# Kernel optimization log

Hardware: AMD Instinct MI355X
Metric: run time of the kernel (lower is better)

The kernel has to match this reference:

```python
import jax, jax.numpy as jnp
import numpy as np

N_NODES = 50000
N_EDGES = 800000
NUM_GRAPHS = 512
D_IN = 64
D_H = 64
BN_EPS = 1e-5


def setup_inputs() -> dict:
    key = jax.random.key(0)
    ks = jax.random.split(key, 12)
    x = jax.random.normal(ks[0], (N_NODES, D_IN), dtype=jnp.float32)
    edge_index = jax.random.randint(ks[1], (2, N_EDGES), 0, N_NODES, dtype=jnp.int64)
    batch = jnp.sort(jax.random.randint(ks[2], (N_NODES,), 0, NUM_GRAPHS, dtype=jnp.int64))
    s1 = 1.0 / np.sqrt(D_IN)
    s2 = 1.0 / np.sqrt(D_H)
    s3 = 1.0 / np.sqrt(2 * D_H)
    W1 = jax.random.uniform(ks[3], (D_IN, D_H), jnp.float32, -s1, s1)
    b1 = jax.random.uniform(ks[4], (D_H,), jnp.float32, -s1, s1)
    gamma = jnp.ones((D_H,), jnp.float32)
    beta = jnp.zeros((D_H,), jnp.float32)
    W2 = jax.random.uniform(ks[5], (D_H, D_H), jnp.float32, -s2, s2)
    b2 = jax.random.uniform(ks[6], (D_H,), jnp.float32, -s2, s2)
    Wl1 = jax.random.uniform(ks[7], (2 * D_H, 2 * D_H), jnp.float32, -s3, s3)
    bl1 = jax.random.uniform(ks[8], (2 * D_H,), jnp.float32, -s3, s3)
    Wl2 = jax.random.uniform(ks[9], (2 * D_H, 1), jnp.float32, -s3, s3)
    bl2 = jax.random.uniform(ks[10], (1,), jnp.float32, -s3, s3)
    return {"x": x, "edge_index": edge_index, "batch": batch,
            "W1": W1, "b1": b1, "gamma": gamma, "beta": beta,
            "W2": W2, "b2": b2, "Wl1": Wl1, "bl1": bl1, "Wl2": Wl2, "bl2": bl2}


def reference(x, edge_index, batch, W1, b1, gamma, beta, W2, b2, Wl1, bl1, Wl2, bl2):
    src, dst = edge_index[0], edge_index[1]
    # GINConv with eps=0: (1+eps)*x_i + sum_{j->i} x_j
    agg = x + jax.ops.segment_sum(x[src], dst, num_segments=N_NODES)
    # MLP: Linear -> BatchNorm1d (training stats, biased var) -> ReLU -> Linear -> ReLU
    h = agg @ W1 + b1
    mean = jnp.mean(h, axis=0)
    var = jnp.var(h, axis=0)
    h = (h - mean) * jax.lax.rsqrt(var + BN_EPS) * gamma + beta
    h = jax.nn.relu(h)
    h = jax.nn.relu(h @ W2 + b2)
    # global add/max pooling per graph
    h_add = jax.ops.segment_sum(h, batch, num_segments=NUM_GRAPHS)
    h_max = jax.ops.segment_max(h, batch, num_segments=NUM_GRAPHS)
    g = jnp.concatenate((h_add, h_max), axis=1)  # [G, 2*D_H]
    g = jax.nn.relu(g @ Wl1 + bl1)
    logits = g @ Wl2 + bl2  # [G, 1]
    return (jax.nn.sigmoid(logits), logits)
```

## Files before the change

kernel.cpp:

```cpp
#include <hip/hip_runtime.h>
#include <hip/hip_bf16.h>

#define N_NODES 50000
#define N_EDGES 800000
#define NUM_GRAPHS 512
#define D 64
#define BN_EPS 1e-5f

#define BUK_SHIFT 7
#define BUK_SIZE 128
#define NBUK ((N_NODES + BUK_SIZE - 1) / BUK_SIZE)
#define CHUNK_A 4096
#define NBLK_A ((N_EDGES + CHUNK_A - 1) / CHUNK_A)
#define GBLK ((N_NODES + 63) / 64)
#define SBLK 256

__global__ __launch_bounds__(512) void k_zero(int* __restrict__ bcnt,
                                              int* __restrict__ offs) {
    int t = threadIdx.x;
    for (int j = t; j < NBUK; j += 512) bcnt[j] = 0;
    if (t == 0) offs[N_NODES] = N_EDGES;
}

__global__ __launch_bounds__(256) void k_bhist(const int* __restrict__ ei,
                                               int* __restrict__ bcnt) {
    __shared__ int h[NBUK];
    int t = threadIdx.x;
    for (int j = t; j < NBUK; j += 256) h[j] = 0;
    __syncthreads();
    int e0 = blockIdx.x * CHUNK_A;
#pragma unroll
    for (int i = 0; i < CHUNK_A / 256; i++) {
        int e = e0 + i * 256 + t;
        if (e < N_EDGES) atomicAdd(&h[ei[N_EDGES + e] >> BUK_SHIFT], 1);
    }
    __syncthreads();
    for (int j = t; j < NBUK; j += 256)
        if (h[j]) atomicAdd(&bcnt[j], h[j]);
}

__global__ __launch_bounds__(512) void k_bscan(const int* __restrict__ bcnt,
                                               int* __restrict__ boffs,
                                               int* __restrict__ gcur) {
    __shared__ int sm[512];
    int t = threadIdx.x;
    int v = (t < NBUK) ? bcnt[t] : 0;
    sm[t] = v;
    __syncthreads();
    for (int off = 1; off < 512; off <<= 1) {
        int a = sm[t];
        int u = (t >= off) ? sm[t - off] : 0;
        __syncthreads();
        sm[t] = a + u;
        __syncthreads();
    }
    if (t < NBUK) { int ex = sm[t] - v; boffs[t] = ex; gcur[t] = ex; }
    if (t == 0) boffs[NBUK] = N_EDGES;
}

__global__ __launch_bounds__(256) void k_binA(const int* __restrict__ ei,
                                              int* __restrict__ gcur,
                                              unsigned* __restrict__ pairs) {
    __shared__ int cnt[NBUK];
    __shared__ int base[NBUK];
    int t = threadIdx.x;
    for (int j = t; j < NBUK; j += 256) cnt[j] = 0;
    __syncthreads();
    int e0 = blockIdx.x * CHUNK_A;
    unsigned pd[CHUNK_A / 256];
    int loc[CHUNK_A / 256];
#pragma unroll
    for (int i = 0; i < CHUNK_A / 256; i++) {
        int e = e0 + i * 256 + t;
        pd[i] = 0xFFFFFFFFu;
        if (e < N_EDGES) {
            unsigned s = (unsigned)ei[e];
            unsigned d = (unsigned)ei[N_EDGES + e];
            pd[i] = (d << 16) | s;
            loc[i] = atomicAdd(&cnt[d >> BUK_SHIFT], 1);
        }
    }
    __syncthreads();
    for (int j = t; j < NBUK; j += 256)
        base[j] = cnt[j] ? atomicAdd(&gcur[j], cnt[j]) : 0;
    __syncthreads();
#pragma unroll
    for (int i = 0; i < CHUNK_A / 256; i++) {
        if (pd[i] != 0xFFFFFFFFu) {
            unsigned d = pd[i] >> 16;
            pairs[base[d >> BUK_SHIFT] + loc[i]] =
                ((d & (BUK_SIZE - 1)) << 16) | (pd[i] & 0xFFFFu);
        }
    }
}

__global__ __launch_bounds__(256) void k_sort(const unsigned* __restrict__ pairs,
                                              const int* __restrict__ boffs,
                                              int* __restrict__ offs,
                                              int* __restrict__ esrc) {
    __shared__ int cnt[BUK_SIZE];
    __shared__ int sm[BUK_SIZE];
    __shared__ int cur[BUK_SIZE];
    int b = blockIdx.x, t = threadIdx.x;
    int n0 = b << BUK_SHIFT;
    int nrows = min(BUK_SIZE, N_NODES - n0);
    int e0 = boffs[b], e1 = boffs[b + 1];
    int m = e1 - e0;
    if (t < BUK_SIZE) cnt[t] = 0;
    __syncthreads();
    for (int j = t; j < m; j += 256)
        atomicAdd(&cnt[pairs[e0 + j] >> 16], 1);
    __syncthreads();
    if (t < BUK_SIZE) sm[t] = cnt[t];
    __syncthreads();
    for (int off = 1; off < BUK_SIZE; off <<= 1) {
        int v = 0, u = 0;
        if (t < BUK_SIZE) { v = sm[t]; u = (t >= off) ? sm[t - off] : 0; }
        __syncthreads();
        if (t < BUK_SIZE) sm[t] = v + u;
        __syncthreads();
    }
    if (t < BUK_SIZE) {
        int ex = sm[t] - cnt[t];
        cur[t] = ex;
        if (t < nrows) offs[n0 + t] = e0 + ex;
    }
    __syncthreads();
    for (int j = t; j < m; j += 256) {
        unsigned p = pairs[e0 + j];
        int pos = atomicAdd(&cur[p >> 16], 1);
        esrc[e0 + pos] = (int)(p & 0xFFFFu);
    }
}

__global__ __launch_bounds__(256) void k_gather(const float* __restrict__ x,
                                                const int* __restrict__ offs,
                                                const int* __restrict__ esrc,
                                                float* __restrict__ agg) {
    int wid = (blockIdx.x * 256 + threadIdx.x) >> 6;
    int c = threadIdx.x & 63;
    if (wid >= N_NODES) return;
    int base = offs[wid];
    int end = offs[wid + 1];
    float acc = x[(size_t)wid * D + c];
    int i = base;
    for (; i + 3 < end; i += 4) {
        int s0 = esrc[i], s1 = esrc[i + 1], s2 = esrc[i + 2], s3 = esrc[i + 3];
        float v0 = x[(size_t)s0 * D + c];
        float v1 = x[(size_t)s1 * D + c];
        float v2 = x[(size_t)s2 * D + c];
        float v3 = x[(size_t)s3 * D + c];
        acc += v0; acc += v1; acc += v2; acc += v3;
    }
    for (; i < end; i++) acc += x[(size_t)esrc[i] * D + c];
    agg[(size_t)wid * D + c] = acc;
}

__global__ __launch_bounds__(256) void k_gemm1(const float* __restrict__ agg,
                                               const float* __restrict__ W1,
                                               const float* __restrict__ b1,
                                               float* __restrict__ h) {
    __shared__ float xs[64][65];
    int blk = blockIdx.x, t = threadIdx.x;
    int r0 = blk * 64;
    const float4* a4 = (const float4*)(agg + (size_t)r0 * D);
    for (int i = t; i < 1024; i += 256) {
        float4 v = a4[i];
        int row = i >> 4, q = (i & 15) * 4;
        xs[row][q] = v.x; xs[row][q + 1] = v.y;
        xs[row][q + 2] = v.z; xs[row][q + 3] = v.w;
    }
    __syncthreads();
    int lane = t & 63, chunk = t >> 6;
    int r = r0 + lane;
    int c0 = chunk * 16;
    float acc[16];
#pragma unroll
    for (int j = 0; j < 16; j++) acc[j] = b1[c0 + j];
#pragma unroll 4
    for (int k = 0; k < D; k++) {
        float v = xs[lane][k];
#pragma unroll
        for (int j = 0; j < 16; j++)
            acc[j] += v * W1[k * D + c0 + j];
    }
    if (r < N_NODES) {
        float* hp = h + (size_t)r * D + c0;
#pragma unroll
        for (int j4 = 0; j4 < 4; j4++) {
            float4 o;
            o.x = acc[j4 * 4]; o.y = acc[j4 * 4 + 1];
            o.z = acc[j4 * 4 + 2]; o.w = acc[j4 * 4 + 3];
            *(float4*)(hp + j4 * 4) = o;
        }
    }
}

__global__ __launch_bounds__(256) void k_bnstats(const float* __restrict__ h,
                                                 float* __restrict__ partial) {
    int t = threadIdx.x, w = t >> 6, c = t & 63;
    float s = 0.f, q = 0.f;
    for (int n = blockIdx.x * 4 + w; n < N_NODES; n += SBLK * 4) {
        float v = h[(size_t)n * D + c];
        s += v; q += v * v;
    }
    __shared__ float shS[4][64], shQ[4][64];
    shS[w][c] = s; shQ[w][c] = q;
    __syncthreads();
    if (w == 0) {
        float ts = shS[0][c] + shS[1][c] + shS[2][c] + shS[3][c];
        float tq = shQ[0][c] + shQ[1][c] + shQ[2][c] + shQ[3][c];
        partial[blockIdx.x * 128 + c] = ts;
        partial[blockIdx.x * 128 + 64 + c] = tq;
    }
}

__global__ __launch_bounds__(512) void k_bnfinal(const float* __restrict__ partial,
                                                 const float* __restrict__ gamma,
                                                 const float* __restrict__ beta,
                                                 float* __restrict__ bnscale,
                                                 float* __restrict__ bnshift) {
    __shared__ float sh[4][128];
    __shared__ float tot[128];
    int t = threadIdx.x, c = t & 127, sl = t >> 7;
    float s = 0.f;
    for (int b = sl; b < SBLK; b += 4) s += partial[b * 128 + c];
    sh[sl][c] = s;
    __syncthreads();
    if (t < 128) tot[t] = sh[0][t] + sh[1][t] + sh[2][t] + sh[3][t];
    __syncthreads();
    if (t < 64) {
        float mean = tot[t] * (1.0f / N_NODES);
        float var  = tot[64 + t] * (1.0f / N_NODES) - mean * mean;
        float rstd = rsqrtf(var + BN_EPS);
        float sc = gamma[t] * rstd;
        bnscale[t] = sc;
        bnshift[t] = beta[t] - mean * sc;
    }
}

__global__ __launch_bounds__(256) void k_gemm2(const float* __restrict__ h,
                                               const float* __restrict__ bnscale,
                                               const float* __restrict__ bnshift,
                                               const float* __restrict__ W2,
                                               const float* __restrict__ b2,
                                               float* __restrict__ h2) {
    __shared__ float xs[64][65];
    __shared__ float bs[64], bb[64];
    int blk = blockIdx.x, t = threadIdx.x;
    if (t < 64) { bs[t] = bnscale[t]; bb[t] = bnshift[t]; }
    __syncthreads();
    int r0 = blk * 64;
    const float4* a4 = (const float4*)(h + (size_t)r0 * D);
    for (int i = t; i < 1024; i += 256) {
        float4 v = a4[i];
        int row = i >> 4, q = (i & 15) * 4;
        xs[row][q]     = fmaxf(v.x * bs[q]     + bb[q],     0.0f);
        xs[row][q + 1] = fmaxf(v.y * bs[q + 1] + bb[q + 1], 0.0f);
        xs[row][q + 2] = fmaxf(v.z * bs[q + 2] + bb[q + 2], 0.0f);
        xs[row][q + 3] = fmaxf(v.w * bs[q + 3] + bb[q + 3], 0.0f);
    }
    __syncthreads();
    int lane = t & 63, chunk = t >> 6;
    int r = r0 + lane;
    int c0 = chunk * 16;
    float acc[16];
#pragma unroll
    for (int j = 0; j < 16; j++) acc[j] = b2[c0 + j];
#pragma unroll 4
    for (int k = 0; k < D; k++) {
        float v = xs[lane][k];
#pragma unroll
        for (int j = 0; j < 16; j++)
            acc[j] += v * W2[k * D + c0 + j];
    }
    if (r < N_NODES) {
        float* hp = h2 + (size_t)r * D + c0;
#pragma unroll
        for (int j4 = 0; j4 < 4; j4++) {
            float4 o;
            o.x = fmaxf(acc[j4 * 4], 0.0f);     o.y = fmaxf(acc[j4 * 4 + 1], 0.0f);
            o.z = fmaxf(acc[j4 * 4 + 2], 0.0f); o.w = fmaxf(acc[j4 * 4 + 3], 0.0f);
            *(float4*)(hp + j4 * 4) = o;
        }
    }
}

__device__ __forceinline__ int lower_bound(const int* __restrict__ b, int v) {
    int lo = 0, hi = N_NODES;
    while (lo < hi) {
        int m = (lo + hi) >> 1;
        if (b[m] < v) lo = m + 1; else hi = m;
    }
    return lo;
}

__global__ __launch_bounds__(256) void k_pool(const float* __restrict__ h2,
                                              const int* __restrict__ batch,
                                              float* __restrict__ g) {
    int gi = blockIdx.x, t = threadIdx.x, w = t >> 6, c = t & 63;
    int s0 = lower_bound(batch, gi);
    int s1 = lower_bound(batch, gi + 1);
    float sm = 0.f, mx = 0.f;
    for (int n = s0 + w; n < s1; n += 4) {
        float v = h2[(size_t)n * D + c];
        sm += v; mx = fmaxf(mx, v);
    }
    __shared__ float shS[4][64], shM[4][64];
    shS[w][c] = sm; shM[w][c] = mx;
    __syncthreads();
    if (w == 0) {
        float ts = shS[0][c] + shS[1][c] + shS[2][c] + shS[3][c];
        float tm = fmaxf(fmaxf(shM[0][c], shM[1][c]), fmaxf(shM[2][c], shM[3][c]));
        g[gi * 128 + c] = ts;
        g[gi * 128 + 64 + c] = tm;
    }
}

__global__ __launch_bounds__(128) void k_head(const float* __restrict__ g,
                                              const float* __restrict__ Wl1,
                                              const float* __restrict__ bl1,
                                              const float* __restrict__ Wl2,
                                              const float* __restrict__ bl2,
                                              float* __restrict__ out) {
    __shared__ float gv[128];
    __shared__ float red[2];
    int gi = blockIdx.x;
    int t = threadIdx.x;
    gv[t] = g[gi * 128 + t];
    __syncthreads();
    float acc = bl1[t];
#pragma unroll
    for (int k = 0; k < 128; k++)
        acc += gv[k] * Wl1[k * 128 + t];
    acc = fmaxf(acc, 0.0f);
    float part = acc * Wl2[t];
    for (int off = 32; off; off >>= 1) part += __shfl_down(part, off);
    if ((t & 63) == 0) red[t >> 6] = part;
    __syncthreads();
    if (t == 0) {
        float logit = red[0] + red[1] + bl2[0];
        out[gi] = 1.0f / (1.0f + expf(-logit));
        out[NUM_GRAPHS + gi] = logit;
    }
}

extern "C" void kernel_launch(void* const* d_in, const int* in_sizes, int n_in,
                              void* d_out, int out_size, void* d_ws, size_t ws_size,
                              hipStream_t stream) {
    const float* x     = (const float*)d_in[0];
    const int*   ei    = (const int*)d_in[1];
    const int*   batch = (const int*)d_in[2];
    const float* W1    = (const float*)d_in[3];
    const float* b1    = (const float*)d_in[4];
    const float* gamma = (const float*)d_in[5];
    const float* beta  = (const float*)d_in[6];
    const float* W2    = (const float*)d_in[7];
    const float* b2    = (const float*)d_in[8];
    const float* Wl1   = (const float*)d_in[9];
    const float* bl1   = (const float*)d_in[10];
    const float* Wl2   = (const float*)d_in[11];
    const float* bl2   = (const float*)d_in[12];
    float* out = (float*)d_out;

    float* ws = (float*)d_ws;
    float* agg    = ws;
    float* h      = agg + (size_t)N_NODES * D;
    float* gbuf   = h + (size_t)N_NODES * D;
    float* bnscale= gbuf + NUM_GRAPHS * 128;
    float* bnshift= bnscale + 64;
    int*   bcnt   = (int*)(bnshift + 64);
    int*   boffs  = bcnt + NBUK;
    int*   gcur   = boffs + NBUK + 1;
    int*   offs   = gcur + NBUK;
    int*   esrc   = offs + N_NODES + 1;
    float* partial= (float*)(esrc + N_EDGES);
    unsigned* pairs = (unsigned*)h;
    float* h2     = agg;

    k_zero   <<<1, 512, 0, stream>>>(bcnt, offs);
    k_bhist  <<<NBLK_A, 256, 0, stream>>>(ei, bcnt);
    k_bscan  <<<1, 512, 0, stream>>>(bcnt, boffs, gcur);
    k_binA   <<<NBLK_A, 256, 0, stream>>>(ei, gcur, pairs);
    k_sort   <<<NBUK, 256, 0, stream>>>(pairs, boffs, offs, esrc);
    k_gather <<<(N_NODES * 64 + 255) / 256, 256, 0, stream>>>(x, offs, esrc, agg);
    k_gemm1  <<<GBLK, 256, 0, stream>>>(agg, W1, b1, h);
    k_bnstats<<<SBLK, 256, 0, stream>>>(h, partial);
    k_bnfinal<<<1, 512, 0, stream>>>(partial, gamma, beta, bnscale, bnshift);
    k_gemm2  <<<GBLK, 256, 0, stream>>>(h, bnscale, bnshift, W2, b2, h2);
    k_pool   <<<NUM_GRAPHS, 256, 0, stream>>>(h2, batch, gbuf);
    k_head   <<<NUM_GRAPHS, 128, 0, stream>>>(gbuf, Wl1, bl1, Wl2, bl2, out);
}
```

Baseline: 277.9 us.

## Fuse BN stats into GEMM1, pooling into GEMM2, vectorize gather

BatchNorm partial statistics are now computed inside the first GEMM from its shared-memory tile, and the second GEMM pools its own output per graph using atomic sum and atomic max, so the separate stats and pool kernels and the h2 round trip through memory go away. The gather kernel now has each wavefront handle four edges at a time with float4 loads and combines them with cross-lane shuffles. The zero kernel is replaced by memsets plus a write in the scan kernel. In exchange, the pooling relies on atomics into a zeroed buffer, and the float atomicMax on int bits is correct only because values are non-negative after ReLU.

```diff
diff --git a/kernel.cpp b/kernel.cpp
--- a/kernel.cpp
+++ b/kernel.cpp
@@ -13,14 +13,6 @@
 #define CHUNK_A 4096
 #define NBLK_A ((N_EDGES + CHUNK_A - 1) / CHUNK_A)
 #define GBLK ((N_NODES + 63) / 64)
-#define SBLK 256
-
-__global__ __launch_bounds__(512) void k_zero(int* __restrict__ bcnt,
-                                              int* __restrict__ offs) {
-    int t = threadIdx.x;
-    for (int j = t; j < NBUK; j += 512) bcnt[j] = 0;
-    if (t == 0) offs[N_NODES] = N_EDGES;
-}
 
 __global__ __launch_bounds__(256) void k_bhist(const int* __restrict__ ei,
                                                int* __restrict__ bcnt) {
@@ -41,7 +33,8 @@
 
 __global__ __launch_bounds__(512) void k_bscan(const int* __restrict__ bcnt,
                                                int* __restrict__ boffs,
-                                               int* __restrict__ gcur) {
+                                               int* __restrict__ gcur,
+                                               int* __restrict__ offs) {
     __shared__ int sm[512];
     int t = threadIdx.x;
     int v = (t < NBUK) ? bcnt[t] : 0;
@@ -55,7 +48,7 @@
         __syncthreads();
     }
     if (t < NBUK) { int ex = sm[t] - v; boffs[t] = ex; gcur[t] = ex; }
-    if (t == 0) boffs[NBUK] = N_EDGES;
+    if (t == 0) { boffs[NBUK] = N_EDGES; offs[N_NODES] = N_EDGES; }
 }
 
 __global__ __launch_bounds__(256) void k_binA(const int* __restrict__ ei,
@@ -138,29 +131,51 @@
                                                 const int* __restrict__ esrc,
                                                 float* __restrict__ agg) {
     int wid = (blockIdx.x * 256 + threadIdx.x) >> 6;
-    int c = threadIdx.x & 63;
+    int lane = threadIdx.x & 63;
     if (wid >= N_NODES) return;
-    int base = offs[wid];
-    int end = offs[wid + 1];
-    float acc = x[(size_t)wid * D + c];
+    int grp = lane >> 4;
+    int f4  = lane & 15;
+    const float4* x4 = (const float4*)x;
+    int base = offs[wid], end = offs[wid + 1];
+    float4 acc = make_float4(0.f, 0.f, 0.f, 0.f);
     int i = base;
+    for (; i + 7 < end; i += 8) {
+        int s0 = esrc[i + grp];
+        int s1 = esrc[i + 4 + grp];
+        float4 v0 = x4[(size_t)s0 * 16 + f4];
+        float4 v1 = x4[(size_t)s1 * 16 + f4];
+        acc.x += v0.x; acc.y += v0.y; acc.z += v0.z; acc.w += v0.w;
+        acc.x += v1.x; acc.y += v1.y; acc.z += v1.z; acc.w += v1.w;
+    }
     for (; i + 3 < end; i += 4) {
-        int s0 = esrc[i], s1 = esrc[i + 1], s2 = esrc[i + 2], s3 = esrc[i + 3];
-        float v0 = x[(size_t)s0 * D + c];
-        float v1 = x[(size_t)s1 * D + c];
-        float v2 = x[(size_t)s2 * D + c];
-        float v3 = x[(size_t)s3 * D + c];
-        acc += v0; acc += v1; acc += v2; acc += v3;
-    }
-    for (; i < end; i++) acc += x[(size_t)esrc[i] * D + c];
-    agg[(size_t)wid * D + c] = acc;
+        int s = esrc[i + grp];
+        float4 v = x4[(size_t)s * 16 + f4];
+        acc.x += v.x; acc.y += v.y; acc.z += v.z; acc.w += v.w;
+    }
+    int rem = end - i;
+    if (grp < rem) {
+        int s = esrc[i + grp];
+        float4 v = x4[(size_t)s * 16 + f4];
+        acc.x += v.x; acc.y += v.y; acc.z += v.z; acc.w += v.w;
+    }
+    acc.x += __shfl_xor(acc.x, 16, 64); acc.y += __shfl_xor(acc.y, 16, 64);
+    acc.z += __shfl_xor(acc.z, 16, 64); acc.w += __shfl_xor(acc.w, 16, 64);
+    acc.x += __shfl_xor(acc.x, 32, 64); acc.y += __shfl_xor(acc.y, 32, 64);
+    acc.z += __shfl_xor(acc.z, 32, 64); acc.w += __shfl_xor(acc.w, 32, 64);
+    if (grp == 0) {
+        float4 xn = x4[(size_t)wid * 16 + f4];
+        acc.x += xn.x; acc.y += xn.y; acc.z += xn.z; acc.w += xn.w;
+        ((float4*)agg)[(size_t)wid * 16 + f4] = acc;
+    }
 }
 
 __global__ __launch_bounds__(256) void k_gemm1(const float* __restrict__ agg,
                                                const float* __restrict__ W1,
                                                const float* __restrict__ b1,
-                                               float* __restrict__ h) {
+                                               float* __restrict__ h,
+                                               float* __restrict__ partial) {
     __shared__ float xs[64][65];
+    __shared__ float shS[4][64], shQ[4][64];
     int blk = blockIdx.x, t = threadIdx.x;
     int r0 = blk * 64;
     const float4* a4 = (const float4*)(agg + (size_t)r0 * D);
@@ -172,8 +187,7 @@
     }
     __syncthreads();
     int lane = t & 63, chunk = t >> 6;
-    int r = r0 + lane;
-    int c0 = chunk * 16;
+    int r = r0 + lane, c0 = chunk * 16;
     float acc[16];
 #pragma unroll
     for (int j = 0; j < 16; j++) acc[j] = b1[c0 + j];
@@ -194,24 +208,25 @@
             *(float4*)(hp + j4 * 4) = o;
         }
     }
-}
-
-__global__ __launch_bounds__(256) void k_bnstats(const float* __restrict__ h,
-                                                 float* __restrict__ partial) {
-    int t = threadIdx.x, w = t >> 6, c = t & 63;
-    float s = 0.f, q = 0.f;
-    for (int n = blockIdx.x * 4 + w; n < N_NODES; n += SBLK * 4) {
-        float v = h[(size_t)n * D + c];
-        s += v; q += v * v;
-    }
-    __shared__ float shS[4][64], shQ[4][64];
-    shS[w][c] = s; shQ[w][c] = q;
-    __syncthreads();
-    if (w == 0) {
-        float ts = shS[0][c] + shS[1][c] + shS[2][c] + shS[3][c];
-        float tq = shQ[0][c] + shQ[1][c] + shQ[2][c] + shQ[3][c];
-        partial[blockIdx.x * 128 + c] = ts;
-        partial[blockIdx.x * 128 + 64 + c] = tq;
+    __syncthreads();
+#pragma unroll
+    for (int j = 0; j < 16; j++) xs[lane][c0 + j] = acc[j];
+    __syncthreads();
+    int nval = min(64, N_NODES - r0);
+    {
+        float s = 0.f, q = 0.f;
+        for (int rr = chunk; rr < nval; rr += 4) {
+            float v = xs[rr][lane];
+            s += v; q += v * v;
+        }
+        shS[chunk][lane] = s; shQ[chunk][lane] = q;
+    }
+    __syncthreads();
+    if (chunk == 0) {
+        float ts = shS[0][lane] + shS[1][lane] + shS[2][lane] + shS[3][lane];
+        float tq = shQ[0][lane] + shQ[1][lane] + shQ[2][lane] + shQ[3][lane];
+        partial[blk * 128 + lane] = ts;
+        partial[blk * 128 + 64 + lane] = tq;
     }
 }
 
@@ -221,17 +236,16 @@
                                                  float* __restrict__ bnscale,
                                                  float* __restrict__ bnshift) {
     __shared__ float sh[4][128];
-    __shared__ float tot[128];
     int t = threadIdx.x, c = t & 127, sl = t >> 7;
     float s = 0.f;
-    for (int b = sl; b < SBLK; b += 4) s += partial[b * 128 + c];
+    for (int b = sl; b < GBLK; b += 4) s += partial[b * 128 + c];
     sh[sl][c] = s;
     __syncthreads();
-    if (t < 128) tot[t] = sh[0][t] + sh[1][t] + sh[2][t] + sh[3][t];
+    if (t < 128) sh[0][t] = sh[0][t] + sh[1][t] + sh[2][t] + sh[3][t];
     __syncthreads();
     if (t < 64) {
-        float mean = tot[t] * (1.0f / N_NODES);
-        float var  = tot[64 + t] * (1.0f / N_NODES) - mean * mean;
+        float mean = sh[0][t] * (1.0f / N_NODES);
+        float var  = sh[0][64 + t] * (1.0f / N_NODES) - mean * mean;
         float rstd = rsqrtf(var + BN_EPS);
         float sc = gamma[t] * rstd;
         bnscale[t] = sc;
@@ -239,14 +253,25 @@
     }
 }
 
-__global__ __launch_bounds__(256) void k_gemm2(const float* __restrict__ h,
-                                               const float* __restrict__ bnscale,
-                                               const float* __restrict__ bnshift,
-                                               const float* __restrict__ W2,
-                                               const float* __restrict__ b2,
-                                               float* __restrict__ h2) {
+__device__ __forceinline__ int lower_bound(const int* __restrict__ b, int v) {
+    int lo = 0, hi = N_NODES;
+    while (lo < hi) {
+        int m = (lo + hi) >> 1;
+        if (b[m] < v) lo = m + 1; else hi = m;
+    }
+    return lo;
+}
+
+__global__ __launch_bounds__(256) void k_gemm2pool(const float* __restrict__ h,
+                                                   const int* __restrict__ batch,
+                                                   const float* __restrict__ bnscale,
+                                                   const float* __restrict__ bnshift,
+                                                   const float* __restrict__ W2,
+                                                   const float* __restrict__ b2,
+                                                   float* __restrict__ g) {
     __shared__ float xs[64][65];
     __shared__ float bs[64], bb[64];
+    __shared__ float shS[4][64], shM[4][64];
     int blk = blockIdx.x, t = threadIdx.x;
     if (t < 64) { bs[t] = bnscale[t]; bb[t] = bnshift[t]; }
     __syncthreads();
@@ -261,9 +286,7 @@
         xs[row][q + 3] = fmaxf(v.w * bs[q + 3] + bb[q + 3], 0.0f);
     }
     __syncthreads();
-    int lane = t & 63, chunk = t >> 6;
-    int r = r0 + lane;
-    int c0 = chunk * 16;
+    int lane = t & 63, chunk = t >> 6, c0 = chunk * 16;
     float acc[16];
 #pragma unroll
     for (int j = 0; j < 16; j++) acc[j] = b2[c0 + j];
@@ -274,46 +297,33 @@
         for (int j = 0; j < 16; j++)
             acc[j] += v * W2[k * D + c0 + j];
     }
-    if (r < N_NODES) {
-        float* hp = h2 + (size_t)r * D + c0;
-#pragma unroll
-        for (int j4 = 0; j4 < 4; j4++) {
-            float4 o;
-            o.x = fmaxf(acc[j4 * 4], 0.0f);     o.y = fmaxf(acc[j4 * 4 + 1], 0.0f);
-            o.z = fmaxf(acc[j4 * 4 + 2], 0.0f); o.w = fmaxf(acc[j4 * 4 + 3], 0.0f);
-            *(float4*)(hp + j4 * 4) = o;
-        }
-    }
-}
-
-__device__ __forceinline__ int lower_bound(const int* __restrict__ b, int v) {
-    int lo = 0, hi = N_NODES;
-    while (lo < hi) {
-        int m = (lo + hi) >> 1;
-        if (b[m] < v) lo = m + 1; else hi = m;
-    }
-    return lo;
-}
-
-__global__ __launch_bounds__(256) void k_pool(const float* __restrict__ h2,
-                                              const int* __restrict__ batch,
-                                              float* __restrict__ g) {
-    int gi = blockIdx.x, t = threadIdx.x, w = t >> 6, c = t & 63;
-    int s0 = lower_bound(batch, gi);
-    int s1 = lower_bound(batch, gi + 1);
-    float sm = 0.f, mx = 0.f;
-    for (int n = s0 + w; n < s1; n += 4) {
-        float v = h2[(size_t)n * D + c];
-        sm += v; mx = fmaxf(mx, v);
-    }
-    __shared__ float shS[4][64], shM[4][64];
-    shS[w][c] = sm; shM[w][c] = mx;
-    __syncthreads();
-    if (w == 0) {
-        float ts = shS[0][c] + shS[1][c] + shS[2][c] + shS[3][c];
-        float tm = fmaxf(fmaxf(shM[0][c], shM[1][c]), fmaxf(shM[2][c], shM[3][c]));
-        g[gi * 128 + c] = ts;
-        g[gi * 128 + 64 + c] = tm;
+#pragma unroll
+    for (int j = 0; j < 16; j++) acc[j] = fmaxf(acc[j], 0.0f);
+    __syncthreads();
+#pragma unroll
+    for (int j = 0; j < 16; j++) xs[lane][c0 + j] = acc[j];
+    __syncthreads();
+    int nval = min(64, N_NODES - r0);
+    int gi0 = batch[r0];
+    int gi1 = batch[r0 + nval - 1];
+    for (int gi = gi0; gi <= gi1; gi++) {
+        int a = max(lower_bound(batch, gi) - r0, 0);
+        int b = min(lower_bound(batch, gi + 1) - r0, nval);
+        float s = 0.f, m = 0.f;
+        for (int rr = a + chunk; rr < b; rr += 4) {
+            float v = xs[rr][lane];
+            s += v; m = fmaxf(m, v);
+        }
+        shS[chunk][lane] = s; shM[chunk][lane] = m;
+        __syncthreads();
+        if (chunk == 0 && b > a) {
+            float ts = shS[0][lane] + shS[1][lane] + shS[2][lane] + shS[3][lane];
+            float tm = fmaxf(fmaxf(shM[0][lane], shM[1][lane]),
+                             fmaxf(shM[2][lane], shM[3][lane]));
+            atomicAdd(&g[gi * 128 + lane], ts);
+            atomicMax((int*)&g[gi * 128 + 64 + lane], __float_as_int(tm));
+        }
+        __syncthreads();
     }
 }
 
@@ -376,18 +386,16 @@
     int*   esrc   = offs + N_NODES + 1;
     float* partial= (float*)(esrc + N_EDGES);
     unsigned* pairs = (unsigned*)h;
-    float* h2     = agg;
-
-    k_zero   <<<1, 512, 0, stream>>>(bcnt, offs);
-    k_bhist  <<<NBLK_A, 256, 0, stream>>>(ei, bcnt);
-    k_bscan  <<<1, 512, 0, stream>>>(bcnt, boffs, gcur);
-    k_binA   <<<NBLK_A, 256, 0, stream>>>(ei, gcur, pairs);
-    k_sort   <<<NBUK, 256, 0, stream>>>(pairs, boffs, offs, esrc);
-    k_gather <<<(N_NODES * 64 + 255) / 256, 256, 0, stream>>>(x, offs, esrc, agg);
-    k_gemm1  <<<GBLK, 256, 0, stream>>>(agg, W1, b1, h);
-    k_bnstats<<<SBLK, 256, 0, stream>>>(h, partial);
-    k_bnfinal<<<1, 512, 0, stream>>>(partial, gamma, beta, bnscale, bnshift);
-    k_gemm2  <<<GBLK, 256, 0, stream>>>(h, bnscale, bnshift, W2, b2, h2);
-    k_pool   <<<NUM_GRAPHS, 256, 0, stream>>>(h2, batch, gbuf);
-    k_head   <<<NUM_GRAPHS, 128, 0, stream>>>(gbuf, Wl1, bl1, Wl2, bl2, out);
-}
+
+    hipMemsetAsync(bcnt, 0, NBUK * sizeof(int), stream);
+    hipMemsetAsync(gbuf, 0, NUM_GRAPHS * 128 * sizeof(float), stream);
+    k_bhist    <<<NBLK_A, 256, 0, stream>>>(ei, bcnt);
+    k_bscan    <<<1, 512, 0, stream>>>(bcnt, boffs, gcur, offs);
+    k_binA     <<<NBLK_A, 256, 0, stream>>>(ei, gcur, pairs);
+    k_sort     <<<NBUK, 256, 0, stream>>>(pairs, boffs, offs, esrc);
+    k_gather   <<<(N_NODES * 64 + 255) / 256, 256, 0, stream>>>(x, offs, esrc, agg);
+    k_gemm1    <<<GBLK, 256, 0, stream>>>(agg, W1, b1, h, partial);
+    k_bnfinal  <<<1, 512, 0, stream>>>(partial, gamma, beta, bnscale, bnshift);
+    k_gemm2pool<<<GBLK, 256, 0, stream>>>(h, batch, bnscale, bnshift, W2, b2, gbuf);
+    k_head     <<<NUM_GRAPHS, 128, 0, stream>>>(gbuf, Wl1, bl1, Wl2, bl2, out);
+}
```

Result: no change. 282.0 us (+1.5%).
